# Optimization experiments

Measured on AMD Instinct MI355X. Metric: run time of the kernel, lower is better.

## Reference

```python
import jax, jax.numpy as jnp
import numpy as np

T, B, I = 1000, 16, 440   # time, batch, input feat
H, P = 1024, 512          # cell size, projection size


def setup_inputs() -> dict:
    key = jax.random.key(0)
    ks = jax.random.split(key, 14)
    s_in = 1.0 / np.sqrt(I)
    s_p = 1.0 / np.sqrt(P)
    s_h = 1.0 / np.sqrt(H)
    inp = {
        "x": jax.random.normal(ks[0], (T, B, I), jnp.float32),
        # input->gate linears (bias=True since no batchnorm/laynorm)
        "wfx_w": jax.random.uniform(ks[1], (H, I), jnp.float32, -s_in, s_in),
        "wfx_b": jax.random.uniform(ks[2], (H,), jnp.float32, -s_in, s_in),
        "wix_w": jax.random.uniform(ks[3], (H, I), jnp.float32, -s_in, s_in),
        "wix_b": jax.random.uniform(ks[4], (H,), jnp.float32, -s_in, s_in),
        "wox_w": jax.random.uniform(ks[5], (H, I), jnp.float32, -s_in, s_in),
        "wox_b": jax.random.uniform(ks[6], (H,), jnp.float32, -s_in, s_in),
        "wcx_w": jax.random.uniform(ks[7], (H, I), jnp.float32, -s_in, s_in),
        "wcx_b": jax.random.uniform(ks[8], (H,), jnp.float32, -s_in, s_in),
        # recurrent projections (bias=False)
        "tfy_w": jax.random.uniform(ks[9], (H, P), jnp.float32, -s_p, s_p),
        "tiy_w": jax.random.uniform(ks[10], (H, P), jnp.float32, -s_p, s_p),
        "toy_w": jax.random.uniform(ks[11], (H, P), jnp.float32, -s_p, s_p),
        "tcy_w": jax.random.uniform(ks[12], (H, P), jnp.float32, -s_p, s_p),
        # output projection h -> y (bias=False)
        "wym_w": jax.random.uniform(ks[13], (P, H), jnp.float32, -s_h, s_h),
    }
    return inp


def reference(x, wfx_w, wfx_b, wix_w, wix_b, wox_w, wox_b, wcx_w, wcx_b,
              tfy_w, tiy_w, toy_w, tcy_w, wym_w):
    # Precompute input-to-gate projections for all timesteps: [T,B,H]
    gf = jnp.einsum('tbi,hi->tbh', x, wfx_w) + wfx_b
    gi = jnp.einsum('tbi,hi->tbh', x, wix_w) + wix_b
    go = jnp.einsum('tbi,hi->tbh', x, wox_w) + wox_b
    gc = jnp.einsum('tbi,hi->tbh', x, wcx_w) + wcx_b

    b = x.shape[1]
    c0 = jnp.zeros((b, H), x.dtype)  # h_init in source (used as cell state)
    y0 = jnp.zeros((b, P), x.dtype)
    drop_mask = jnp.asarray(1.0, x.dtype)  # test mode: 1 - drop, drop=0.0

    def step(carry, g):
        ct, yt = carry
        gf_t, gi_t, go_t, gc_t = g
        it = jax.nn.sigmoid(gi_t + yt @ tiy_w.T)
        ft = jax.nn.sigmoid(gf_t + yt @ tfy_w.T)
        ot = jax.nn.sigmoid(go_t + yt @ toy_w.T)
        ct = it * jnp.tanh(gc_t + yt @ tcy_w.T) * drop_mask + ft * ct
        ht = ot * jnp.tanh(ct)
        yt = ht @ wym_w.T
        return (ct, yt), ht

    _, h = jax.lax.scan(step, (c0, y0), (gf, gi, go, gc))
    return h  # [T, B, H]
```

## Files before the change

kernel.cpp:

```cpp
#include <hip/hip_runtime.h>
#include <hip/hip_fp16.h>
#include <stdint.h>

#define T_STEPS 1000
#define BATCH   16
#define IFEAT   440
#define KPAD    448
#define HDIM    1024
#define PDIM    512
#define NWG     64

typedef _Float16 f16x8 __attribute__((ext_vector_type(8)));
typedef _Float16 f16x4 __attribute__((ext_vector_type(4)));
typedef float    f32x4 __attribute__((ext_vector_type(4)));
typedef uint32_t u32x4 __attribute__((ext_vector_type(4)));

union F16x8U { f16x8 v; u32x4 w; };

#define OFF_HB    0u
#define OFF_XH    65536u
#define OFF_W4    (OFF_XH + 14336000u)
#define OFF_TG    (OFF_W4 + 3670016u)
#define OFF_WYT   (OFF_TG + 4194304u)
#define OFF_M     (OFF_WYT + 1048576u)
#define OFF_GX    (OFF_M + 8388608u)

__device__ __forceinline__ float sigm_(float x)  { return 1.f / (1.f + __expf(-x)); }
__device__ __forceinline__ float tanh_(float x)  { return 1.f - 2.f / (1.f + __expf(2.f * x)); }

__global__ void init_hb(unsigned short* __restrict__ HB) {
    int i = blockIdx.x * 256 + threadIdx.x;
    HB[i] = (i < BATCH * HDIM) ? (unsigned short)0x0000 : (unsigned short)0x0001;
}

__global__ void prep_x(const float* __restrict__ x, _Float16* __restrict__ xh) {
    int idx = blockIdx.x * 256 + threadIdx.x;
    const int total = T_STEPS * BATCH * KPAD;
    for (; idx < total; idx += gridDim.x * 256) {
        int k = idx % KPAD;
        int row = idx / KPAD;
        float v = (k < IFEAT) ? x[row * IFEAT + k] : 0.f;
        xh[idx] = (_Float16)v;
    }
}

__global__ void prep_w(const float* __restrict__ wi, const float* __restrict__ wf,
                       const float* __restrict__ wo, const float* __restrict__ wc,
                       const float* __restrict__ ti, const float* __restrict__ tf,
                       const float* __restrict__ to_, const float* __restrict__ tc,
                       const float* __restrict__ wym,
                       _Float16* __restrict__ W4, _Float16* __restrict__ TG,
                       _Float16* __restrict__ WYT) {
    int tid = blockIdx.x * 256 + threadIdx.x;
    int stride = gridDim.x * 256;
    const float* const Wsrc[4] = {wi, wf, wo, wc};
    const float* const Tsrc[4] = {ti, tf, to_, tc};
    const int totW = 4 * HDIM * KPAD;
    for (int idx = tid; idx < totW; idx += stride) {
        int k = idx % KPAD; int gh = idx / KPAD;
        int h = gh % HDIM;  int g = gh / HDIM;
        W4[idx] = (_Float16)((k < IFEAT) ? Wsrc[g][h * IFEAT + k] : 0.f);
    }
    const int totT = 4 * HDIM * PDIM;
    for (int idx = tid; idx < totT; idx += stride) {
        int p = idx % PDIM; int gh = idx / PDIM;
        int h = gh % HDIM;  int g = gh / HDIM;
        TG[idx] = (_Float16)Tsrc[g][h * PDIM + p];
    }
    const int totY = HDIM * PDIM;
    for (int idx = tid; idx < totY; idx += stride) {
        int p = idx % PDIM; int hh = idx / PDIM;
        WYT[idx] = (_Float16)wym[p * HDIM + hh];
    }
}

__global__ __launch_bounds__(256) void mgemm(const _Float16* __restrict__ TG,
                                             const _Float16* __restrict__ WYT,
                                             _Float16* __restrict__ M) {
    int wave = threadIdx.x >> 6, l = threadIdx.x & 63;
    int lo = l & 15, quad = l >> 4;
    int tile = blockIdx.x * 4 + wave;
    int g = tile >> 12;
    int ht = (tile >> 6) & 63;
    int hht = tile & 63;
    const _Float16* Ar = TG  + ((size_t)(g * HDIM + ht * 16 + lo)) * PDIM;
    const _Float16* Br = WYT + ((size_t)(hht * 16 + lo)) * PDIM;
    f32x4 acc = {0.f, 0.f, 0.f, 0.f};
#pragma unroll
    for (int cc = 0; cc < 16; ++cc) {
        f16x8 a = *(const f16x8*)(Ar + cc * 32 + quad * 8);
        f16x8 b = *(const f16x8*)(Br + cc * 32 + quad * 8);
        acc = __builtin_amdgcn_mfma_f32_16x16x32_f16(a, b, acc, 0, 0, 0);
    }
    _Float16* dst = M + (size_t)g * HDIM * HDIM;
#pragma unroll
    for (int r = 0; r < 4; ++r)
        dst[(size_t)(ht * 16 + quad * 4 + r) * HDIM + hht * 16 + lo] = (_Float16)acc[r];
}

#define TT 4
__global__ __launch_bounds__(256) void phase1(const _Float16* __restrict__ xh,
                                              const _Float16* __restrict__ W4,
                                              const float* __restrict__ bI,
                                              const float* __restrict__ bF,
                                              const float* __restrict__ bO,
                                              const float* __restrict__ bC,
                                              _Float16* __restrict__ GX) {
    __shared__ _Float16 sx[TT * 16 * 456];
    const int t0 = blockIdx.x * TT;
    for (int c = threadIdx.x; c < TT * 16 * 56; c += 256) {
        int kc = c % 56, rowi = c / 56;
        *(f16x8*)(sx + rowi * 456 + kc * 8) =
            *(const f16x8*)(xh + ((size_t)(t0 * 16 + rowi)) * KPAD + kc * 8);
    }
    __syncthreads();
    const int wave = threadIdx.x >> 6, l = threadIdx.x & 63;
    const int lo = l & 15, quad = l >> 4;
    const int g = wave;
    const float* bias = (g == 0) ? bI : (g == 1) ? bF : (g == 2) ? bO : bC;
    for (int htp = 0; htp < 32; ++htp) {
        const int ht0 = htp * 2, ht1 = htp * 2 + 1;
        f16x8 A0[14], A1[14];
        const _Float16* Ar0 = W4 + ((size_t)(g * HDIM + ht0 * 16 + lo)) * KPAD;
        const _Float16* Ar1 = Ar0 + (size_t)16 * KPAD;
#pragma unroll
        for (int cc = 0; cc < 14; ++cc) {
            A0[cc] = *(const f16x8*)(Ar0 + cc * 32 + quad * 8);
            A1[cc] = *(const f16x8*)(Ar1 + cc * 32 + quad * 8);
        }
        float b0[4], b1[4];
#pragma unroll
        for (int r = 0; r < 4; ++r) {
            b0[r] = bias[ht0 * 16 + quad * 4 + r];
            b1[r] = bias[ht1 * 16 + quad * 4 + r];
        }
        for (int t = 0; t < TT; ++t) {
            f32x4 acc0 = {0.f, 0.f, 0.f, 0.f}, acc1 = {0.f, 0.f, 0.f, 0.f};
#pragma unroll
            for (int cc = 0; cc < 14; ++cc) {
                f16x8 b = *(const f16x8*)(sx + (t * 16 + lo) * 456 + cc * 32 + quad * 8);
                acc0 = __builtin_amdgcn_mfma_f32_16x16x32_f16(A0[cc], b, acc0, 0, 0, 0);
                acc1 = __builtin_amdgcn_mfma_f32_16x16x32_f16(A1[cc], b, acc1, 0, 0, 0);
            }
            size_t tbase = ((size_t)(t0 + t) * 4 + g) * 64;
            f16x4 h0, h1;
#pragma unroll
            for (int r = 0; r < 4; ++r) {
                h0[r] = (_Float16)(acc0[r] + b0[r]);
                h1[r] = (_Float16)(acc1[r] + b1[r]);
            }
            *(f16x4*)(GX + ((tbase + ht0) * 64 + l) * 4) = h0;
            *(f16x4*)(GX + ((tbase + ht1) * 64 + l) * 4) = h1;
        }
    }
}

__global__ __launch_bounds__(256, 1) void recur(const _Float16* __restrict__ GX,
                                                const _Float16* __restrict__ Mw,
                                                _Float16* __restrict__ HB,
                                                float* __restrict__ out) {
    const int tid = threadIdx.x, wave = tid >> 6, l = tid & 63;
    const int lo = l & 15, quad = l >> 4;
    const int ht = blockIdx.x;
    const int kbase = wave * 256;

    f16x8 A[4][8];
#pragma unroll
    for (int g = 0; g < 4; ++g) {
        const _Float16* Ar = Mw + ((size_t)g * HDIM + ht * 16 + lo) * HDIM + kbase;
#pragma unroll
        for (int cc = 0; cc < 8; ++cc)
            A[g][cc] = *(const f16x8*)(Ar + cc * 32 + quad * 8);
    }

    __shared__ float P[2][4][4][64][4];
    f32x4 ct = {0.f, 0.f, 0.f, 0.f};

    f16x4 gxbuf[2][4];
    if (wave < 2) {
#pragma unroll
        for (int g = 0; g < 4; ++g) {
            gxbuf[0][g] = *(const f16x4*)(GX + ((((size_t)0 * 4 + g) * 64 + ht) * 64 + l) * 4);
            gxbuf[1][g] = *(const f16x4*)(GX + ((((size_t)1 * 4 + g) * 64 + ht) * 64 + l) * 4);
        }
    }

    const _Float16* hb0 = HB + (size_t)lo * HDIM + kbase + quad * 8;
    _Float16* hs0 = HB + (size_t)lo * HDIM + ht * 16 + quad * 4;

    auto step = [&](int t, int slot) {
        const int par = t & 1;
        const uint32_t expw = ((t >> 1) & 1) ? 0x00010001u : 0u;
        const uint64_t pollA = (uint64_t)(uintptr_t)(hb0 + (size_t)par * BATCH * HDIM);

        F16x8U B[8];
        while (true) {
            asm volatile(
                "global_load_dwordx4 %0, %8, off sc0 sc1\n\t"
                "global_load_dwordx4 %1, %8, off offset:64 sc0 sc1\n\t"
                "global_load_dwordx4 %2, %8, off offset:128 sc0 sc1\n\t"
                "global_load_dwordx4 %3, %8, off offset:192 sc0 sc1\n\t"
                "global_load_dwordx4 %4, %8, off offset:256 sc0 sc1\n\t"
                "global_load_dwordx4 %5, %8, off offset:320 sc0 sc1\n\t"
                "global_load_dwordx4 %6, %8, off offset:384 sc0 sc1\n\t"
                "global_load_dwordx4 %7, %8, off offset:448 sc0 sc1\n\t"
                "s_waitcnt vmcnt(0)"
                : "=&v"(B[0].w), "=&v"(B[1].w), "=&v"(B[2].w), "=&v"(B[3].w),
                  "=&v"(B[4].w), "=&v"(B[5].w), "=&v"(B[6].w), "=&v"(B[7].w)
                : "v"(pollA)
                : "memory");
            uint32_t bad = 0;
#pragma unroll
            for (int c = 0; c < 8; ++c)
#pragma unroll
                for (int j = 0; j < 4; ++j)
                    bad |= (B[c].w[j] ^ expw) & 0x00010001u;
            if (__all(bad == 0)) break;
        }

        f32x4 acc[4];
#pragma unroll
        for (int g = 0; g < 4; ++g) acc[g] = (f32x4){0.f, 0.f, 0.f, 0.f};
#pragma unroll
        for (int cc = 0; cc < 8; ++cc) {
#pragma unroll
            for (int g = 0; g < 4; ++g)
                acc[g] = __builtin_amdgcn_mfma_f32_16x16x32_f16(A[g][cc], B[cc].v, acc[g], 0, 0, 0);
        }
#pragma unroll
        for (int g = 0; g < 4; ++g)
            *(f32x4*)&P[par][wave][g][l][0] = acc[g];
        __syncthreads();

        if (wave < 2) {
            f32x4 pre[4];
#pragma unroll
            for (int g = 0; g < 4; ++g) {
                f32x4 s = *(const f32x4*)&P[par][0][g][l][0];
#pragma unroll
                for (int k = 1; k < 4; ++k) s = s + *(const f32x4*)&P[par][k][g][l][0];
                f16x4 gv = gxbuf[slot][g];
#pragma unroll
                for (int r = 0; r < 4; ++r) s[r] += (float)gv[r];
                pre[g] = s;
            }
            f32x4 hv; f16x4 hh;
#pragma unroll
            for (int r = 0; r < 4; ++r) {
                float it = sigm_(pre[0][r]);
                float ft = sigm_(pre[1][r]);
                float ot = sigm_(pre[2][r]);
                float gt = tanh_(pre[3][r]);
                ct[r] = it * gt + ft * ct[r];
                float h = ot * tanh_(ct[r]);
                hv[r] = h; hh[r] = (_Float16)h;
            }
            if (wave == 0) {
                unsigned long long bits; __builtin_memcpy(&bits, &hh, 8);
                const unsigned long long TAG = 0x0001000100010001ULL;
                unsigned long long genw = (unsigned long long)(((t + 1) >> 1) & 1);
                bits = (bits & ~TAG) | (genw * TAG);
                uint64_t sA = (uint64_t)(uintptr_t)(hs0 + (size_t)((t + 1) & 1) * BATCH * HDIM);
                asm volatile("global_store_dwordx2 %0, %1, off sc0 sc1"
                             :: "v"(sA), "v"(bits) : "memory");
            } else {
                __builtin_nontemporal_store(hv,
                    (f32x4*)(out + ((size_t)t * BATCH + lo) * HDIM + ht * 16 + quad * 4));
            }
            int tp = (t + 2 < T_STEPS) ? (t + 2) : (T_STEPS - 1);
#pragma unroll
            for (int g = 0; g < 4; ++g)
                gxbuf[slot][g] = *(const f16x4*)(GX + ((((size_t)tp * 4 + g) * 64 + ht) * 64 + l) * 4);
        }
    };

    for (int t = 0; t < T_STEPS; t += 2) {
        step(t, 0);
        step(t + 1, 1);
    }
}

extern "C" void kernel_launch(void* const* d_in, const int* in_sizes, int n_in,
                              void* d_out, int out_size, void* d_ws, size_t ws_size,
                              hipStream_t stream) {
    const float* x    = (const float*)d_in[0];
    const float* wfxw = (const float*)d_in[1];
    const float* wfxb = (const float*)d_in[2];
    const float* wixw = (const float*)d_in[3];
    const float* wixb = (const float*)d_in[4];
    const float* woxw = (const float*)d_in[5];
    const float* woxb = (const float*)d_in[6];
    const float* wcxw = (const float*)d_in[7];
    const float* wcxb = (const float*)d_in[8];
    const float* tfyw = (const float*)d_in[9];
    const float* tiyw = (const float*)d_in[10];
    const float* toyw = (const float*)d_in[11];
    const float* tcyw = (const float*)d_in[12];
    const float* wymw = (const float*)d_in[13];

    char* ws = (char*)d_ws;
    _Float16*  HB    = (_Float16*)(ws + OFF_HB);
    _Float16*  XH    = (_Float16*)(ws + OFF_XH);
    _Float16*  W4    = (_Float16*)(ws + OFF_W4);
    _Float16*  TG    = (_Float16*)(ws + OFF_TG);
    _Float16*  WYT   = (_Float16*)(ws + OFF_WYT);
    _Float16*  Mw    = (_Float16*)(ws + OFF_M);
    _Float16*  GX    = (_Float16*)(ws + OFF_GX);
    float* out = (float*)d_out;

    init_hb<<<128, 256, 0, stream>>>((unsigned short*)HB);
    prep_x<<<4096, 256, 0, stream>>>(x, XH);
    prep_w<<<2048, 256, 0, stream>>>(wixw, wfxw, woxw, wcxw,
                                     tiyw, tfyw, toyw, tcyw, wymw,
                                     W4, TG, WYT);
    mgemm<<<4096, 256, 0, stream>>>(TG, WYT, Mw);
    phase1<<<250, 256, 0, stream>>>(XH, W4, wixb, wfxb, woxb, wcxb, GX);
    recur<<<NWG, 256, 0, stream>>>(GX, Mw, HB, out);
}
```

Baseline: 4.733 ms.

## Add dedicated epilogue wave and poll two tags before selective reload

The recurrent kernel gets a fifth wave that does only the gate nonlinearities, the h store and the gx prefetch, so the four MFMA waves do nothing but poll and multiply. Polling now reads two probe vectors until their tags match, then loads the full h slice and re-issues only the chunks whose tags are still stale, instead of reloading all eight chunks on every spin. This aims to cut memory traffic during the spin-wait and take epilogue work off the critical MFMA waves. In exchange, the single epilogue wave does work that two waves shared before, which may lengthen the serial tail of each step.

```diff
diff --git a/kernel.cpp b/kernel.cpp
--- a/kernel.cpp
+++ b/kernel.cpp
@@ -155,7 +155,7 @@
     }
 }
 
-__global__ __launch_bounds__(256, 1) void recur(const _Float16* __restrict__ GX,
+__global__ __launch_bounds__(320, 1) void recur(const _Float16* __restrict__ GX,
                                                 const _Float16* __restrict__ Mw,
                                                 _Float16* __restrict__ HB,
                                                 float* __restrict__ out) {
@@ -165,19 +165,21 @@
     const int kbase = wave * 256;
 
     f16x8 A[4][8];
-#pragma unroll
-    for (int g = 0; g < 4; ++g) {
-        const _Float16* Ar = Mw + ((size_t)g * HDIM + ht * 16 + lo) * HDIM + kbase;
-#pragma unroll
-        for (int cc = 0; cc < 8; ++cc)
-            A[g][cc] = *(const f16x8*)(Ar + cc * 32 + quad * 8);
+    if (wave < 4) {
+#pragma unroll
+        for (int g = 0; g < 4; ++g) {
+            const _Float16* Ar = Mw + ((size_t)g * HDIM + ht * 16 + lo) * HDIM + kbase;
+#pragma unroll
+            for (int cc = 0; cc < 8; ++cc)
+                A[g][cc] = *(const f16x8*)(Ar + cc * 32 + quad * 8);
+        }
     }
 
     __shared__ float P[2][4][4][64][4];
     f32x4 ct = {0.f, 0.f, 0.f, 0.f};
 
     f16x4 gxbuf[2][4];
-    if (wave < 2) {
+    if (wave == 4) {
 #pragma unroll
         for (int g = 0; g < 4; ++g) {
             gxbuf[0][g] = *(const f16x4*)(GX + ((((size_t)0 * 4 + g) * 64 + ht) * 64 + l) * 4);
@@ -191,48 +193,69 @@
     auto step = [&](int t, int slot) {
         const int par = t & 1;
         const uint32_t expw = ((t >> 1) & 1) ? 0x00010001u : 0u;
-        const uint64_t pollA = (uint64_t)(uintptr_t)(hb0 + (size_t)par * BATCH * HDIM);
-
-        F16x8U B[8];
-        while (true) {
-            asm volatile(
-                "global_load_dwordx4 %0, %8, off sc0 sc1\n\t"
-                "global_load_dwordx4 %1, %8, off offset:64 sc0 sc1\n\t"
-                "global_load_dwordx4 %2, %8, off offset:128 sc0 sc1\n\t"
-                "global_load_dwordx4 %3, %8, off offset:192 sc0 sc1\n\t"
-                "global_load_dwordx4 %4, %8, off offset:256 sc0 sc1\n\t"
-                "global_load_dwordx4 %5, %8, off offset:320 sc0 sc1\n\t"
-                "global_load_dwordx4 %6, %8, off offset:384 sc0 sc1\n\t"
-                "global_load_dwordx4 %7, %8, off offset:448 sc0 sc1\n\t"
-                "s_waitcnt vmcnt(0)"
-                : "=&v"(B[0].w), "=&v"(B[1].w), "=&v"(B[2].w), "=&v"(B[3].w),
-                  "=&v"(B[4].w), "=&v"(B[5].w), "=&v"(B[6].w), "=&v"(B[7].w)
-                : "v"(pollA)
-                : "memory");
-            uint32_t bad = 0;
-#pragma unroll
-            for (int c = 0; c < 8; ++c)
-#pragma unroll
-                for (int j = 0; j < 4; ++j)
-                    bad |= (B[c].w[j] ^ expw) & 0x00010001u;
-            if (__all(bad == 0)) break;
-        }
-
-        f32x4 acc[4];
-#pragma unroll
-        for (int g = 0; g < 4; ++g) acc[g] = (f32x4){0.f, 0.f, 0.f, 0.f};
-#pragma unroll
-        for (int cc = 0; cc < 8; ++cc) {
+
+        if (wave < 4) {
+            const uint64_t pollA = (uint64_t)(uintptr_t)(hb0 + (size_t)par * BATCH * HDIM);
+
+            while (true) {
+                u32x4 s0, s1;
+                asm volatile(
+                    "global_load_dwordx4 %0, %2, off sc0 sc1\n\t"
+                    "global_load_dwordx4 %1, %2, off offset:256 sc0 sc1\n\t"
+                    "s_waitcnt vmcnt(0)"
+                    : "=&v"(s0), "=&v"(s1) : "v"(pollA) : "memory");
+                uint32_t bad = 0;
+#pragma unroll
+                for (int j = 0; j < 4; ++j) {
+                    bad |= (s0[j] ^ expw) & 0x00010001u;
+                    bad |= (s1[j] ^ expw) & 0x00010001u;
+                }
+                if (__all(bad == 0)) break;
+            }
+
+            F16x8U B[8];
+            uint32_t pend = 0xFFu;
+            do {
+                if (pend & 0x01u) asm volatile("global_load_dwordx4 %0, %1, off sc0 sc1"            : "=&v"(B[0].w) : "v"(pollA) : "memory");
+                if (pend & 0x02u) asm volatile("global_load_dwordx4 %0, %1, off offset:64 sc0 sc1"  : "=&v"(B[1].w) : "v"(pollA) : "memory");
+                if (pend & 0x04u) asm volatile("global_load_dwordx4 %0, %1, off offset:128 sc0 sc1" : "=&v"(B[2].w) : "v"(pollA) : "memory");
+                if (pend & 0x08u) asm volatile("global_load_dwordx4 %0, %1, off offset:192 sc0 sc1" : "=&v"(B[3].w) : "v"(pollA) : "memory");
+                if (pend & 0x10u) asm volatile("global_load_dwordx4 %0, %1, off offset:256 sc0 sc1" : "=&v"(B[4].w) : "v"(pollA) : "memory");
+                if (pend & 0x20u) asm volatile("global_load_dwordx4 %0, %1, off offset:320 sc0 sc1" : "=&v"(B[5].w) : "v"(pollA) : "memory");
+                if (pend & 0x40u) asm volatile("global_load_dwordx4 %0, %1, off offset:384 sc0 sc1" : "=&v"(B[6].w) : "v"(pollA) : "memory");
+                if (pend & 0x80u) asm volatile("global_load_dwordx4 %0, %1, off offset:448 sc0 sc1" : "=&v"(B[7].w) : "v"(pollA) : "memory");
+                asm volatile("s_waitcnt vmcnt(0)"
+                             : "+v"(B[0].w), "+v"(B[1].w), "+v"(B[2].w), "+v"(B[3].w),
+                               "+v"(B[4].w), "+v"(B[5].w), "+v"(B[6].w), "+v"(B[7].w)
+                             :: "memory");
+                uint32_t np = 0;
+#pragma unroll
+                for (int c = 0; c < 8; ++c) {
+                    uint32_t bad = 0;
+#pragma unroll
+                    for (int j = 0; j < 4; ++j) bad |= (B[c].w[j] ^ expw) & 0x00010001u;
+                    if (!__all(bad == 0)) np |= (1u << c);
+                }
+                pend = np;
+            } while (pend);
+
+            f32x4 acc[4];
+#pragma unroll
+            for (int g = 0; g < 4; ++g) acc[g] = (f32x4){0.f, 0.f, 0.f, 0.f};
+#pragma unroll
+            for (int cc = 0; cc < 8; ++cc) {
+#pragma unroll
+                for (int g = 0; g < 4; ++g)
+                    acc[g] = __builtin_amdgcn_mfma_f32_16x16x32_f16(A[g][cc], B[cc].v, acc[g], 0, 0, 0);
+            }
 #pragma unroll
             for (int g = 0; g < 4; ++g)
-                acc[g] = __builtin_amdgcn_mfma_f32_16x16x32_f16(A[g][cc], B[cc].v, acc[g], 0, 0, 0);
-        }
-#pragma unroll
-        for (int g = 0; g < 4; ++g)
-            *(f32x4*)&P[par][wave][g][l][0] = acc[g];
+                *(f32x4*)&P[par][wave][g][l][0] = acc[g];
+        }
+
         __syncthreads();
 
-        if (wave < 2) {
+        if (wave == 4) {
             f32x4 pre[4];
 #pragma unroll
             for (int g = 0; g < 4; ++g) {
@@ -255,18 +278,15 @@
                 float h = ot * tanh_(ct[r]);
                 hv[r] = h; hh[r] = (_Float16)h;
             }
-            if (wave == 0) {
-                unsigned long long bits; __builtin_memcpy(&bits, &hh, 8);
-                const unsigned long long TAG = 0x0001000100010001ULL;
-                unsigned long long genw = (unsigned long long)(((t + 1) >> 1) & 1);
-                bits = (bits & ~TAG) | (genw * TAG);
-                uint64_t sA = (uint64_t)(uintptr_t)(hs0 + (size_t)((t + 1) & 1) * BATCH * HDIM);
-                asm volatile("global_store_dwordx2 %0, %1, off sc0 sc1"
-                             :: "v"(sA), "v"(bits) : "memory");
-            } else {
-                __builtin_nontemporal_store(hv,
-                    (f32x4*)(out + ((size_t)t * BATCH + lo) * HDIM + ht * 16 + quad * 4));
-            }
+            unsigned long long bits; __builtin_memcpy(&bits, &hh, 8);
+            const unsigned long long TAG = 0x0001000100010001ULL;
+            unsigned long long genw = (unsigned long long)(((t + 1) >> 1) & 1);
+            bits = (bits & ~TAG) | (genw * TAG);
+            uint64_t sA = (uint64_t)(uintptr_t)(hs0 + (size_t)((t + 1) & 1) * BATCH * HDIM);
+            asm volatile("global_store_dwordx2 %0, %1, off sc0 sc1"
+                         :: "v"(sA), "v"(bits) : "memory");
+            __builtin_nontemporal_store(hv,
+                (f32x4*)(out + ((size_t)t * BATCH + lo) * HDIM + ht * 16 + quad * 4));
             int tp = (t + 2 < T_STEPS) ? (t + 2) : (T_STEPS - 1);
 #pragma unroll
             for (int g = 0; g < 4; ++g)
@@ -315,5 +335,5 @@
                                      W4, TG, WYT);
     mgemm<<<4096, 256, 0, stream>>>(TG, WYT, Mw);
     phase1<<<250, 256, 0, stream>>>(XH, W4, wixb, wfxb, woxb, wcxb, GX);
-    recur<<<NWG, 256, 0, stream>>>(GX, Mw, HB, out);
-}
+    recur<<<NWG, 320, 0, stream>>>(GX, Mw, HB, out);
+}
```

Measured after the change: 5.047 ms. +6.6%, slower.

## Replace tag-bit polling on h buffer with a global atomic step counter

Applied to the files above, without the earlier changes.

Drops the scheme where the lowest bit of each fp16 h value served as a generation tag that consumers polled on. Instead, each workgroup bumps a single global counter with an atomic after storing its h slice, and all workgroups spin on that counter reaching 64*t before doing a plain load of h. This removes the tag-bit precision loss and the repeated 8x16B data polls. In exchange it adds a serial atomic and a second dependent memory round trip per step, all aimed at one hot address. The spin also has an iteration cap that could let a workgroup read stale data.

```diff
diff --git a/kernel.cpp b/kernel.cpp
--- a/kernel.cpp
+++ b/kernel.cpp
@@ -30,7 +30,11 @@
 
 __global__ void init_hb(unsigned short* __restrict__ HB) {
     int i = blockIdx.x * 256 + threadIdx.x;
-    HB[i] = (i < BATCH * HDIM) ? (unsigned short)0x0000 : (unsigned short)0x0001;
+    HB[i] = 0;
+}
+
+__global__ void init_sync(int* __restrict__ S) {
+    if (threadIdx.x < 32) S[threadIdx.x] = 0;
 }
 
 __global__ void prep_x(const float* __restrict__ x, _Float16* __restrict__ xh) {
@@ -158,7 +162,8 @@
 __global__ __launch_bounds__(256, 1) void recur(const _Float16* __restrict__ GX,
                                                 const _Float16* __restrict__ Mw,
                                                 _Float16* __restrict__ HB,
-                                                float* __restrict__ out) {
+                                                float* __restrict__ out,
+                                                int* __restrict__ SYNC) {
     const int tid = threadIdx.x, wave = tid >> 6, l = tid & 63;
     const int lo = l & 15, quad = l >> 4;
     const int ht = blockIdx.x;
@@ -187,36 +192,38 @@
 
     const _Float16* hb0 = HB + (size_t)lo * HDIM + kbase + quad * 8;
     _Float16* hs0 = HB + (size_t)lo * HDIM + ht * 16 + quad * 4;
-
-    auto step = [&](int t, int slot) {
+    const uint64_t cntA = (uint64_t)(uintptr_t)SYNC;
+
+    for (int t = 0; t < T_STEPS; ++t) {
         const int par = t & 1;
-        const uint32_t expw = ((t >> 1) & 1) ? 0x00010001u : 0u;
-        const uint64_t pollA = (uint64_t)(uintptr_t)(hb0 + (size_t)par * BATCH * HDIM);
-
+
+        if (t > 0) {
+            const int want = 64 * t;
+            int c, spins = 0;
+            do {
+                asm volatile("global_load_dword %0, %1, off sc0 sc1\n\t"
+                             "s_waitcnt vmcnt(0)"
+                             : "=v"(c) : "v"(cntA) : "memory");
+                if (++spins > (1 << 20)) break;
+            } while (c < want);
+        }
+
+        const uint64_t bA = (uint64_t)(uintptr_t)(hb0 + (size_t)par * BATCH * HDIM);
         F16x8U B[8];
-        while (true) {
-            asm volatile(
-                "global_load_dwordx4 %0, %8, off sc0 sc1\n\t"
-                "global_load_dwordx4 %1, %8, off offset:64 sc0 sc1\n\t"
-                "global_load_dwordx4 %2, %8, off offset:128 sc0 sc1\n\t"
-                "global_load_dwordx4 %3, %8, off offset:192 sc0 sc1\n\t"
-                "global_load_dwordx4 %4, %8, off offset:256 sc0 sc1\n\t"
-                "global_load_dwordx4 %5, %8, off offset:320 sc0 sc1\n\t"
-                "global_load_dwordx4 %6, %8, off offset:384 sc0 sc1\n\t"
-                "global_load_dwordx4 %7, %8, off offset:448 sc0 sc1\n\t"
-                "s_waitcnt vmcnt(0)"
-                : "=&v"(B[0].w), "=&v"(B[1].w), "=&v"(B[2].w), "=&v"(B[3].w),
-                  "=&v"(B[4].w), "=&v"(B[5].w), "=&v"(B[6].w), "=&v"(B[7].w)
-                : "v"(pollA)
-                : "memory");
-            uint32_t bad = 0;
-#pragma unroll
-            for (int c = 0; c < 8; ++c)
-#pragma unroll
-                for (int j = 0; j < 4; ++j)
-                    bad |= (B[c].w[j] ^ expw) & 0x00010001u;
-            if (__all(bad == 0)) break;
-        }
+        asm volatile(
+            "global_load_dwordx4 %0, %8, off sc0 sc1\n\t"
+            "global_load_dwordx4 %1, %8, off offset:64 sc0 sc1\n\t"
+            "global_load_dwordx4 %2, %8, off offset:128 sc0 sc1\n\t"
+            "global_load_dwordx4 %3, %8, off offset:192 sc0 sc1\n\t"
+            "global_load_dwordx4 %4, %8, off offset:256 sc0 sc1\n\t"
+            "global_load_dwordx4 %5, %8, off offset:320 sc0 sc1\n\t"
+            "global_load_dwordx4 %6, %8, off offset:384 sc0 sc1\n\t"
+            "global_load_dwordx4 %7, %8, off offset:448 sc0 sc1\n\t"
+            "s_waitcnt vmcnt(0)"
+            : "=&v"(B[0].w), "=&v"(B[1].w), "=&v"(B[2].w), "=&v"(B[3].w),
+              "=&v"(B[4].w), "=&v"(B[5].w), "=&v"(B[6].w), "=&v"(B[7].w)
+            : "v"(bA)
+            : "memory");
 
         f32x4 acc[4];
 #pragma unroll
@@ -230,6 +237,7 @@
 #pragma unroll
         for (int g = 0; g < 4; ++g)
             *(f32x4*)&P[par][wave][g][l][0] = acc[g];
+
         __syncthreads();
 
         if (wave < 2) {
@@ -239,7 +247,7 @@
                 f32x4 s = *(const f32x4*)&P[par][0][g][l][0];
 #pragma unroll
                 for (int k = 1; k < 4; ++k) s = s + *(const f32x4*)&P[par][k][g][l][0];
-                f16x4 gv = gxbuf[slot][g];
+                f16x4 gv = gxbuf[par][g];
 #pragma unroll
                 for (int r = 0; r < 4; ++r) s[r] += (float)gv[r];
                 pre[g] = s;
@@ -257,12 +265,11 @@
             }
             if (wave == 0) {
                 unsigned long long bits; __builtin_memcpy(&bits, &hh, 8);
-                const unsigned long long TAG = 0x0001000100010001ULL;
-                unsigned long long genw = (unsigned long long)(((t + 1) >> 1) & 1);
-                bits = (bits & ~TAG) | (genw * TAG);
-                uint64_t sA = (uint64_t)(uintptr_t)(hs0 + (size_t)((t + 1) & 1) * BATCH * HDIM);
+                const uint64_t sA = (uint64_t)(uintptr_t)(hs0 + (size_t)((t + 1) & 1) * BATCH * HDIM);
                 asm volatile("global_store_dwordx2 %0, %1, off sc0 sc1"
                              :: "v"(sA), "v"(bits) : "memory");
+                asm volatile("s_waitcnt vmcnt(0)" ::: "memory");
+                if (l == 0) atomicAdd(SYNC, 1);
             } else {
                 __builtin_nontemporal_store(hv,
                     (f32x4*)(out + ((size_t)t * BATCH + lo) * HDIM + ht * 16 + quad * 4));
@@ -270,13 +277,8 @@
             int tp = (t + 2 < T_STEPS) ? (t + 2) : (T_STEPS - 1);
 #pragma unroll
             for (int g = 0; g < 4; ++g)
-                gxbuf[slot][g] = *(const f16x4*)(GX + ((((size_t)tp * 4 + g) * 64 + ht) * 64 + l) * 4);
-        }
-    };
-
-    for (int t = 0; t < T_STEPS; t += 2) {
-        step(t, 0);
-        step(t + 1, 1);
+                gxbuf[par][g] = *(const f16x4*)(GX + ((((size_t)tp * 4 + g) * 64 + ht) * 64 + l) * 4);
+        }
     }
 }
 
@@ -301,6 +303,7 @@
     char* ws = (char*)d_ws;
     _Float16*  HB    = (_Float16*)(ws + OFF_HB);
     _Float16*  XH    = (_Float16*)(ws + OFF_XH);
+    int*       SYNC  = (int*)(ws + OFF_XH);
     _Float16*  W4    = (_Float16*)(ws + OFF_W4);
     _Float16*  TG    = (_Float16*)(ws + OFF_TG);
     _Float16*  WYT   = (_Float16*)(ws + OFF_WYT);
@@ -315,5 +318,6 @@
                                      W4, TG, WYT);
     mgemm<<<4096, 256, 0, stream>>>(TG, WYT, Mw);
     phase1<<<250, 256, 0, stream>>>(XH, W4, wixb, wfxb, woxb, wcxb, GX);
-    recur<<<NWG, 256, 0, stream>>>(GX, Mw, HB, out);
-}
+    init_sync<<<1, 64, 0, stream>>>(SYNC);
+    recur<<<NWG, 256, 0, stream>>>(GX, Mw, HB, out, SYNC);
+}
```

New measurement: 13.28 ms. 181% more time.

## Add helper wave for GX prefetch and output stores in recurrent kernel

Applied to the files above, without the earlier changes.

Adds a fifth wave per workgroup that prefetches the input-gate projections into a shared ring buffer and writes the fp32 hidden outputs to global memory. The four compute waves now only poll, run the MFMAs, and perform the gate math on wave 0. The goal is to take global loads and stores off the critical recurrent path. In exchange it adds shared-memory flag handshakes with sleep loops and an extra barrier per step. Those could add latency, and the synchronisation between the two sides looks fragile.

```diff
diff --git a/kernel.cpp b/kernel.cpp
--- a/kernel.cpp
+++ b/kernel.cpp
@@ -155,107 +155,114 @@
     }
 }
 
-__global__ __launch_bounds__(256, 1) void recur(const _Float16* __restrict__ GX,
+__global__ __launch_bounds__(320, 1) void recur(const _Float16* __restrict__ GX,
                                                 const _Float16* __restrict__ Mw,
                                                 _Float16* __restrict__ HB,
                                                 float* __restrict__ out) {
     const int tid = threadIdx.x, wave = tid >> 6, l = tid & 63;
     const int lo = l & 15, quad = l >> 4;
     const int ht = blockIdx.x;
-    const int kbase = wave * 256;
-
-    f16x8 A[4][8];
-#pragma unroll
-    for (int g = 0; g < 4; ++g) {
-        const _Float16* Ar = Mw + ((size_t)g * HDIM + ht * 16 + lo) * HDIM + kbase;
-#pragma unroll
-        for (int cc = 0; cc < 8; ++cc)
-            A[g][cc] = *(const f16x8*)(Ar + cc * 32 + quad * 8);
-    }
 
     __shared__ float P[2][4][4][64][4];
-    f32x4 ct = {0.f, 0.f, 0.f, 0.f};
-
-    f16x4 gxbuf[2][4];
-    if (wave < 2) {
+    __shared__ f16x4 GXR[4][4][64];
+    __shared__ f32x4 OUTB[64];
+    __shared__ int hvstep_s;
+    __shared__ int gxready_s;
+
+    if (tid == 0) hvstep_s = -1;
+
+    if (wave < 4) {
+        const int kbase = wave * 256;
+
+        f16x8 A[4][8];
 #pragma unroll
         for (int g = 0; g < 4; ++g) {
-            gxbuf[0][g] = *(const f16x4*)(GX + ((((size_t)0 * 4 + g) * 64 + ht) * 64 + l) * 4);
-            gxbuf[1][g] = *(const f16x4*)(GX + ((((size_t)1 * 4 + g) * 64 + ht) * 64 + l) * 4);
-        }
-    }
-
-    const _Float16* hb0 = HB + (size_t)lo * HDIM + kbase + quad * 8;
-    _Float16* hs0 = HB + (size_t)lo * HDIM + ht * 16 + quad * 4;
-
-    auto step = [&](int t, int slot) {
-        const int par = t & 1;
-        const uint32_t expw = ((t >> 1) & 1) ? 0x00010001u : 0u;
-        const uint64_t pollA = (uint64_t)(uintptr_t)(hb0 + (size_t)par * BATCH * HDIM);
-
-        F16x8U B[8];
-        while (true) {
-            asm volatile(
-                "global_load_dwordx4 %0, %8, off sc0 sc1\n\t"
-                "global_load_dwordx4 %1, %8, off offset:64 sc0 sc1\n\t"
-                "global_load_dwordx4 %2, %8, off offset:128 sc0 sc1\n\t"
-                "global_load_dwordx4 %3, %8, off offset:192 sc0 sc1\n\t"
-                "global_load_dwordx4 %4, %8, off offset:256 sc0 sc1\n\t"
-                "global_load_dwordx4 %5, %8, off offset:320 sc0 sc1\n\t"
-                "global_load_dwordx4 %6, %8, off offset:384 sc0 sc1\n\t"
-                "global_load_dwordx4 %7, %8, off offset:448 sc0 sc1\n\t"
-                "s_waitcnt vmcnt(0)"
-                : "=&v"(B[0].w), "=&v"(B[1].w), "=&v"(B[2].w), "=&v"(B[3].w),
-                  "=&v"(B[4].w), "=&v"(B[5].w), "=&v"(B[6].w), "=&v"(B[7].w)
-                : "v"(pollA)
-                : "memory");
-            uint32_t bad = 0;
-#pragma unroll
-            for (int c = 0; c < 8; ++c)
-#pragma unroll
-                for (int j = 0; j < 4; ++j)
-                    bad |= (B[c].w[j] ^ expw) & 0x00010001u;
-            if (__all(bad == 0)) break;
-        }
-
-        f32x4 acc[4];
-#pragma unroll
-        for (int g = 0; g < 4; ++g) acc[g] = (f32x4){0.f, 0.f, 0.f, 0.f};
-#pragma unroll
-        for (int cc = 0; cc < 8; ++cc) {
+            const _Float16* Ar = Mw + ((size_t)g * HDIM + ht * 16 + lo) * HDIM + kbase;
+#pragma unroll
+            for (int cc = 0; cc < 8; ++cc)
+                A[g][cc] = *(const f16x8*)(Ar + cc * 32 + quad * 8);
+        }
+
+        f32x4 ct = {0.f, 0.f, 0.f, 0.f};
+        const _Float16* hb0 = HB + (size_t)lo * HDIM + kbase + quad * 8;
+        _Float16* hs0 = HB + (size_t)lo * HDIM + ht * 16 + quad * 4;
+
+        __syncthreads();
+
+        for (int t = 0; t < T_STEPS; ++t) {
+            const int par = t & 1;
+            const uint32_t expw = ((t >> 1) & 1) ? 0x00010001u : 0u;
+            const uint64_t pollA = (uint64_t)(uintptr_t)(hb0 + (size_t)par * BATCH * HDIM);
+
+            F16x8U B[8];
+            while (true) {
+                asm volatile(
+                    "global_load_dwordx4 %0, %8, off sc0 sc1\n\t"
+                    "global_load_dwordx4 %1, %8, off offset:64 sc0 sc1\n\t"
+                    "global_load_dwordx4 %2, %8, off offset:128 sc0 sc1\n\t"
+                    "global_load_dwordx4 %3, %8, off offset:192 sc0 sc1\n\t"
+                    "global_load_dwordx4 %4, %8, off offset:256 sc0 sc1\n\t"
+                    "global_load_dwordx4 %5, %8, off offset:320 sc0 sc1\n\t"
+                    "global_load_dwordx4 %6, %8, off offset:384 sc0 sc1\n\t"
+                    "global_load_dwordx4 %7, %8, off offset:448 sc0 sc1\n\t"
+                    "s_waitcnt vmcnt(0)"
+                    : "=&v"(B[0].w), "=&v"(B[1].w), "=&v"(B[2].w), "=&v"(B[3].w),
+                      "=&v"(B[4].w), "=&v"(B[5].w), "=&v"(B[6].w), "=&v"(B[7].w)
+                    : "v"(pollA)
+                    : "memory");
+                uint32_t bad = 0;
+#pragma unroll
+                for (int c = 0; c < 8; ++c)
+#pragma unroll
+                    for (int j = 0; j < 4; ++j)
+                        bad |= (B[c].w[j] ^ expw) & 0x00010001u;
+                if (__all(bad == 0)) break;
+            }
+
+            f32x4 acc[4];
+#pragma unroll
+            for (int g = 0; g < 4; ++g) acc[g] = (f32x4){0.f, 0.f, 0.f, 0.f};
+#pragma unroll
+            for (int cc = 0; cc < 8; ++cc) {
+#pragma unroll
+                for (int g = 0; g < 4; ++g)
+                    acc[g] = __builtin_amdgcn_mfma_f32_16x16x32_f16(A[g][cc], B[cc].v, acc[g], 0, 0, 0);
+            }
 #pragma unroll
             for (int g = 0; g < 4; ++g)
-                acc[g] = __builtin_amdgcn_mfma_f32_16x16x32_f16(A[g][cc], B[cc].v, acc[g], 0, 0, 0);
-        }
-#pragma unroll
-        for (int g = 0; g < 4; ++g)
-            *(f32x4*)&P[par][wave][g][l][0] = acc[g];
-        __syncthreads();
-
-        if (wave < 2) {
-            f32x4 pre[4];
-#pragma unroll
-            for (int g = 0; g < 4; ++g) {
-                f32x4 s = *(const f32x4*)&P[par][0][g][l][0];
-#pragma unroll
-                for (int k = 1; k < 4; ++k) s = s + *(const f32x4*)&P[par][k][g][l][0];
-                f16x4 gv = gxbuf[slot][g];
-#pragma unroll
-                for (int r = 0; r < 4; ++r) s[r] += (float)gv[r];
-                pre[g] = s;
-            }
-            f32x4 hv; f16x4 hh;
-#pragma unroll
-            for (int r = 0; r < 4; ++r) {
-                float it = sigm_(pre[0][r]);
-                float ft = sigm_(pre[1][r]);
-                float ot = sigm_(pre[2][r]);
-                float gt = tanh_(pre[3][r]);
-                ct[r] = it * gt + ft * ct[r];
-                float h = ot * tanh_(ct[r]);
-                hv[r] = h; hh[r] = (_Float16)h;
-            }
+                *(f32x4*)&P[par][wave][g][l][0] = acc[g];
+
+            __syncthreads();
+
             if (wave == 0) {
+                f32x4 pre[4];
+#pragma unroll
+                for (int g = 0; g < 4; ++g) {
+                    f32x4 s = *(const f32x4*)&P[par][0][g][l][0];
+#pragma unroll
+                    for (int k = 1; k < 4; ++k) s = s + *(const f32x4*)&P[par][k][g][l][0];
+                    pre[g] = s;
+                }
+                while (__hip_atomic_load(&gxready_s, __ATOMIC_ACQUIRE,
+                                         __HIP_MEMORY_SCOPE_WORKGROUP) < t)
+                    __builtin_amdgcn_s_sleep(1);
+#pragma unroll
+                for (int g = 0; g < 4; ++g) {
+                    f16x4 gv = GXR[t & 3][g][l];
+#pragma unroll
+                    for (int r = 0; r < 4; ++r) pre[g][r] += (float)gv[r];
+                }
+                f32x4 hv; f16x4 hh;
+#pragma unroll
+                for (int r = 0; r < 4; ++r) {
+                    float it = sigm_(pre[0][r]);
+                    float ft = sigm_(pre[1][r]);
+                    float ot = sigm_(pre[2][r]);
+                    float gt = tanh_(pre[3][r]);
+                    ct[r] = it * gt + ft * ct[r];
+                    float h = ot * tanh_(ct[r]);
+                    hv[r] = h; hh[r] = (_Float16)h;
+                }
                 unsigned long long bits; __builtin_memcpy(&bits, &hh, 8);
                 const unsigned long long TAG = 0x0001000100010001ULL;
                 unsigned long long genw = (unsigned long long)(((t + 1) >> 1) & 1);
@@ -263,20 +270,45 @@
                 uint64_t sA = (uint64_t)(uintptr_t)(hs0 + (size_t)((t + 1) & 1) * BATCH * HDIM);
                 asm volatile("global_store_dwordx2 %0, %1, off sc0 sc1"
                              :: "v"(sA), "v"(bits) : "memory");
-            } else {
-                __builtin_nontemporal_store(hv,
-                    (f32x4*)(out + ((size_t)t * BATCH + lo) * HDIM + ht * 16 + quad * 4));
-            }
-            int tp = (t + 2 < T_STEPS) ? (t + 2) : (T_STEPS - 1);
+                OUTB[l] = hv;
+                if (l == 0)
+                    __hip_atomic_store(&hvstep_s, t, __ATOMIC_RELEASE,
+                                       __HIP_MEMORY_SCOPE_WORKGROUP);
+            }
+        }
+    } else {
+        f16x4 G[4];
+#pragma unroll
+        for (int s = 0; s < 2; ++s)
 #pragma unroll
             for (int g = 0; g < 4; ++g)
-                gxbuf[slot][g] = *(const f16x4*)(GX + ((((size_t)tp * 4 + g) * 64 + ht) * 64 + l) * 4);
-        }
-    };
-
-    for (int t = 0; t < T_STEPS; t += 2) {
-        step(t, 0);
-        step(t + 1, 1);
+                GXR[s][g][l] = *(const f16x4*)(GX + ((((size_t)s * 4 + g) * 64 + ht) * 64 + l) * 4);
+#pragma unroll
+        for (int g = 0; g < 4; ++g)
+            G[g] = *(const f16x4*)(GX + ((((size_t)2 * 4 + g) * 64 + ht) * 64 + l) * 4);
+        if (l == 0)
+            __hip_atomic_store(&gxready_s, 1, __ATOMIC_RELEASE,
+                               __HIP_MEMORY_SCOPE_WORKGROUP);
+        __syncthreads();
+
+        for (int t = 0; t < T_STEPS; ++t) {
+            __syncthreads();
+            while (__hip_atomic_load(&hvstep_s, __ATOMIC_ACQUIRE,
+                                     __HIP_MEMORY_SCOPE_WORKGROUP) < t)
+                __builtin_amdgcn_s_sleep(1);
+#pragma unroll
+            for (int g = 0; g < 4; ++g) GXR[(t + 2) & 3][g][l] = G[g];
+            if (l == 0)
+                __hip_atomic_store(&gxready_s, t + 2, __ATOMIC_RELEASE,
+                                   __HIP_MEMORY_SCOPE_WORKGROUP);
+            f32x4 hv = OUTB[l];
+            __builtin_nontemporal_store(hv,
+                (f32x4*)(out + ((size_t)t * BATCH + lo) * HDIM + ht * 16 + quad * 4));
+            int tp = (t + 3 < T_STEPS) ? (t + 3) : (T_STEPS - 1);
+#pragma unroll
+            for (int g = 0; g < 4; ++g)
+                G[g] = *(const f16x4*)(GX + ((((size_t)tp * 4 + g) * 64 + ht) * 64 + l) * 4);
+        }
     }
 }
 
@@ -315,5 +347,5 @@
                                      W4, TG, WYT);
     mgemm<<<4096, 256, 0, stream>>>(TG, WYT, Mw);
     phase1<<<250, 256, 0, stream>>>(XH, W4, wixb, wfxb, woxb, wcxb, GX);
-    recur<<<NWG, 256, 0, stream>>>(GX, Mw, HB, out);
-}
+    recur<<<NWG, 320, 0, stream>>>(GX, Mw, HB, out);
+}
```

Result: faster. 4.593 ms (-3.0%).
